# Optimization experiments

Hardware: AMD Instinct MI355X
Metric: run time of the kernel (lower is better)

Reference implementation:

```python
import jax, jax.numpy as jnp
import numpy as np

N_NODES = 50000
N_EDGES = 800000
D_IN = 256
D_OUT = 256


def setup_inputs() -> dict:
    key = jax.random.key(0)
    ks = jax.random.split(key, 8)
    x = jax.random.normal(ks[0], (N_NODES, D_IN), dtype=jnp.float32)
    edge_index = jax.random.randint(ks[1], (2, N_EDGES), 0, N_NODES, dtype=jnp.int64)
    W_src = jax.random.normal(ks[2], (D_IN, D_OUT), dtype=jnp.float32) * 0.05
    b_src = jax.random.normal(ks[3], (D_OUT,), dtype=jnp.float32) * 0.05
    W_dst = jax.random.normal(ks[4], (D_IN, D_OUT), dtype=jnp.float32) * 0.05
    b_dst = jax.random.normal(ks[5], (D_OUT,), dtype=jnp.float32) * 0.05
    W_self = jax.random.normal(ks[6], (D_IN, D_OUT), dtype=jnp.float32) * 0.05
    b_self = jax.random.normal(ks[7], (D_OUT,), dtype=jnp.float32) * 0.05
    return {"x": x, "edge_index": edge_index, "W_src": W_src, "b_src": b_src,
            "W_dst": W_dst, "b_dst": b_dst, "W_self": W_self, "b_self": b_self}


def reference(x, edge_index, W_src, b_src, W_dst, b_dst, W_self, b_self):
    # LEConv: messages = src_linear(x[row]) - dst_linear(x[col]);
    # scatter-add messages into destination nodes (col); add self_linear(x).
    # Linear commutes with row-gather, so project once on [N, d] then gather.
    row, col = edge_index[0], edge_index[1]
    src = x @ W_src + b_src            # [N, D_OUT]
    dst = x @ W_dst + b_dst            # [N, D_OUT]
    messages = src[row] - dst[col]     # [E, D_OUT]
    agg = jax.ops.segment_sum(messages, col, num_segments=x.shape[0])  # [N, D_OUT]
    return x @ W_self + b_self + agg
```

## Files before the change

kernel.cpp:

```cpp
#include <hip/hip_runtime.h>

#define D 256

typedef unsigned short ushort_t;
typedef unsigned int uint_t;
typedef __attribute__((ext_vector_type(8))) short short8;
typedef __attribute__((ext_vector_type(4))) float floatx4;

static __device__ __forceinline__ ushort_t f2bf(float f) {
    union { float f; uint_t u; } c; c.f = f;
    uint_t r = (c.u + 0x7FFFu + ((c.u >> 16) & 1u)) >> 16;
    return (ushort_t)r;
}
static __device__ __forceinline__ float bf2f(ushort_t b) {
    union { uint_t u; float f; } c; c.u = ((uint_t)b) << 16;
    return c.f;
}

static __device__ __forceinline__ void async16(const void* g, void* l) {
    __builtin_amdgcn_global_load_lds(
        (const __attribute__((address_space(1))) void*)g,
        (__attribute__((address_space(3))) void*)l, 16, 0, 0);
}

__global__ void prep_kernel(const int* __restrict__ col, int* __restrict__ deg,
                            int* __restrict__ rank,
                            const float* __restrict__ x, ushort_t* __restrict__ xh,
                            const float* __restrict__ Wself, const float* __restrict__ Wsrc,
                            const float* __restrict__ Wdst, ushort_t* __restrict__ BT,
                            int E, int total8, int degB, int cvtB) {
    int b = blockIdx.x;
    if (b < degB) {
        int e = b * 256 + threadIdx.x;
        if (e < E) rank[e] = atomicAdd(&deg[col[e]], 1);
    } else if (b < degB + cvtB) {
        int i = (b - degB) * 256 + threadIdx.x;
        if (i >= total8) return;
        float4 a = ((const float4*)x)[i * 2];
        float4 bb = ((const float4*)x)[i * 2 + 1];
        uint4 o;
        o.x = f2bf(a.x) | ((uint_t)f2bf(a.y) << 16);
        o.y = f2bf(a.z) | ((uint_t)f2bf(a.w) << 16);
        o.z = f2bf(bb.x) | ((uint_t)f2bf(bb.y) << 16);
        o.w = f2bf(bb.z) | ((uint_t)f2bf(bb.w) << 16);
        ((uint4*)xh)[i] = o;
    } else {
        int id = (b - degB - cvtB) * 256 + threadIdx.x;
        if (id >= 256 * 768) return;
        int j = id / 768, k = id % 768;
        float v;
        if (k < 256)      v = Wself[(size_t)k * 256 + j];
        else if (k < 512) v = Wsrc [(size_t)(k - 256) * 256 + j];
        else              v = Wdst [(size_t)(k - 512) * 256 + j];
        BT[id] = f2bf(v);
    }
}

__global__ __launch_bounds__(256) void scanA(const int* __restrict__ deg,
                                             int* __restrict__ off,
                                             int* __restrict__ partials, int n4) {
    __shared__ int wtot[4];
    const int tid = threadIdx.x, lane = tid & 63, wid = tid >> 6;
    int i4 = blockIdx.x * 256 + tid;
    int4 v = (i4 < n4) ? ((const int4*)deg)[i4] : make_int4(0, 0, 0, 0);
    int s = v.x + v.y + v.z + v.w;
    int incl = s;
    #pragma unroll
    for (int st = 1; st < 64; st <<= 1) {
        int t = __shfl_up(incl, st, 64);
        if (lane >= st) incl += t;
    }
    if (lane == 63) wtot[wid] = incl;
    __syncthreads();
    int wbase = 0;
    #pragma unroll
    for (int w = 0; w < 4; ++w) if (w < wid) wbase += wtot[w];
    int excl = incl - s + wbase;
    if (i4 < n4) {
        int4 o;
        o.x = excl; o.y = o.x + v.x; o.z = o.y + v.y; o.w = o.z + v.z;
        ((int4*)off)[i4] = o;
    }
    if (tid == 0) partials[blockIdx.x] = wtot[0] + wtot[1] + wtot[2] + wtot[3];
}

__global__ __launch_bounds__(256) void scanC(int* __restrict__ off,
                                             const int* __restrict__ partials, int n4) {
    __shared__ int base_s;
    const int tid = threadIdx.x;
    if (tid < 64) {
        int v = (tid < blockIdx.x) ? partials[tid] : 0;
        #pragma unroll
        for (int st = 32; st; st >>= 1) v += __shfl_down(v, st, 64);
        if (tid == 0) base_s = v;
    }
    __syncthreads();
    int base = base_s;
    int i4 = blockIdx.x * 256 + tid;
    if (i4 < n4) {
        int4 o = ((int4*)off)[i4];
        o.x += base; o.y += base; o.z += base; o.w += base;
        ((int4*)off)[i4] = o;
    }
}

__global__ void fill_kernel(const int* __restrict__ row, const int* __restrict__ col,
                            const int* __restrict__ rank, const int* __restrict__ off,
                            int* __restrict__ bucket, int E) {
    int e = blockIdx.x * blockDim.x + threadIdx.x;
    if (e >= E) return;
    bucket[off[col[e]] + rank[e]] = row[e];
}

__global__ __launch_bounds__(256) void segsum_kernel(const ushort_t* __restrict__ xh,
                                                     const int* __restrict__ off,
                                                     const int* __restrict__ deg,
                                                     const int* __restrict__ bucket,
                                                     ushort_t* __restrict__ Gh, int N) {
    int node = blockIdx.x * 4 + (threadIdx.x >> 6);
    int lane = threadIdx.x & 63;
    if (node >= N) return;
    int start = off[node];
    int cnt = deg[node];
    float a0 = 0.f, a1 = 0.f, a2 = 0.f, a3 = 0.f;
    int i = 0;
    for (; i + 4 <= cnt; i += 4) {
        int r0 = bucket[start + i];
        int r1 = bucket[start + i + 1];
        int r2 = bucket[start + i + 2];
        int r3 = bucket[start + i + 3];
        ushort4 v0 = ((const ushort4*)(xh + (size_t)r0 * D))[lane];
        ushort4 v1 = ((const ushort4*)(xh + (size_t)r1 * D))[lane];
        ushort4 v2 = ((const ushort4*)(xh + (size_t)r2 * D))[lane];
        ushort4 v3 = ((const ushort4*)(xh + (size_t)r3 * D))[lane];
        a0 += (bf2f(v0.x) + bf2f(v1.x)) + (bf2f(v2.x) + bf2f(v3.x));
        a1 += (bf2f(v0.y) + bf2f(v1.y)) + (bf2f(v2.y) + bf2f(v3.y));
        a2 += (bf2f(v0.z) + bf2f(v1.z)) + (bf2f(v2.z) + bf2f(v3.z));
        a3 += (bf2f(v0.w) + bf2f(v1.w)) + (bf2f(v2.w) + bf2f(v3.w));
    }
    for (; i < cnt; ++i) {
        int r0 = bucket[start + i];
        ushort4 v0 = ((const ushort4*)(xh + (size_t)r0 * D))[lane];
        a0 += bf2f(v0.x); a1 += bf2f(v0.y); a2 += bf2f(v0.z); a3 += bf2f(v0.w);
    }
    ushort4 o;
    o.x = f2bf(a0); o.y = f2bf(a1); o.z = f2bf(a2); o.w = f2bf(a3);
    ((ushort4*)(Gh + (size_t)node * D))[lane] = o;
}

__global__ __launch_bounds__(256, 2) void mfma_gemm(
    const ushort_t* __restrict__ xh, const ushort_t* __restrict__ Gh,
    const ushort_t* __restrict__ BT, const int* __restrict__ deg,
    const float* __restrict__ bsrc, const float* __restrict__ bdst,
    const float* __restrict__ bself, float* __restrict__ out, int N)
{
    __shared__ ushort_t Bs[2][16][64][8];
    __shared__ ushort_t Bd[2][16][64][8];

    const int tid = threadIdx.x;
    const int lane = tid & 63, wave = tid >> 6;
    const int quad = lane >> 4, l15 = lane & 15;
    const int wr = wave >> 1, wc = wave & 1;
    const int mbase = blockIdx.x * 128;

    size_t aoff[4];
    float negdeg[4];
    #pragma unroll
    for (int im = 0; im < 4; ++im) {
        int r = mbase + wr * 64 + im * 16 + l15;
        if (r >= N) r = N - 1;
        aoff[im] = (size_t)r * 256 + (size_t)(quad * 8);
        negdeg[im] = -(float)deg[r];
    }

    const ushort_t* bpg[4];
    #pragma unroll
    for (int t = 0; t < 4; ++t)
        bpg[t] = BT + (size_t)((wave * 4 + t) * 16 + l15) * 768 + quad * 8;

    floatx4 acc[4][8] = {};
    short8 af[2][4];

    auto issueB = [&](int s) {
        const int b = s & 1;
        if (s < 8) {
            const int kb = s * 32;
            #pragma unroll
            for (int t = 0; t < 4; ++t)
                async16(bpg[t] + kb, &Bs[b][wave * 4 + t][0][0]);
            #pragma unroll
            for (int t = 0; t < 4; ++t)
                async16(bpg[t] + 512 + kb, &Bd[b][wave * 4 + t][0][0]);
        } else {
            const int kb = 256 + (s - 8) * 32;
            #pragma unroll
            for (int t = 0; t < 4; ++t)
                async16(bpg[t] + kb, &Bs[b][wave * 4 + t][0][0]);
        }
    };
    auto loadA = [&](int s) {
        const ushort_t* Ap = (s < 8) ? xh : Gh;
        const int ka = (s & 7) * 32;
        #pragma unroll
        for (int im = 0; im < 4; ++im)
            af[s & 1][im] = *(const short8*)(Ap + aoff[im] + ka);
    };

    issueB(0);
    loadA(0);

    #pragma unroll
    for (int s = 0; s < 16; ++s) {
        const int cur = s & 1;

        if (s < 15) { issueB(s + 1); loadA(s + 1); }

        if (s < 7)        asm volatile("s_waitcnt vmcnt(12)" ::: "memory");
        else if (s < 15)  asm volatile("s_waitcnt vmcnt(8)"  ::: "memory");
        else              asm volatile("s_waitcnt vmcnt(0)"  ::: "memory");
        __builtin_amdgcn_s_barrier();

        #pragma unroll
        for (int jn = 0; jn < 8; ++jn) {
            short8 bf = *(const short8*)(&Bs[cur][wc * 8 + jn][lane][0]);
            #pragma unroll
            for (int im = 0; im < 4; ++im)
                acc[im][jn] = __builtin_amdgcn_mfma_f32_16x16x32_bf16(
                    af[cur][im], bf, acc[im][jn], 0, 0, 0);
        }
        if (s < 8) {
            short8 afd[4];
            #pragma unroll
            for (int im = 0; im < 4; ++im) {
                short8 t = af[cur][im];
                #pragma unroll
                for (int j = 0; j < 8; ++j) {
                    float f = bf2f((ushort_t)t[j]) * negdeg[im];
                    t[j] = (short)f2bf(f);
                }
                afd[im] = t;
            }
            #pragma unroll
            for (int jn = 0; jn < 8; ++jn) {
                short8 bf = *(const short8*)(&Bd[cur][wc * 8 + jn][lane][0]);
                #pragma unroll
                for (int im = 0; im < 4; ++im)
                    acc[im][jn] = __builtin_amdgcn_mfma_f32_16x16x32_bf16(
                        afd[im], bf, acc[im][jn], 0, 0, 0);
            }
        }

        if (s < 15) __builtin_amdgcn_s_barrier();
    }

    float degv[4][4];
    #pragma unroll
    for (int im = 0; im < 4; ++im)
        #pragma unroll
        for (int r = 0; r < 4; ++r) {
            int gm = mbase + wr * 64 + im * 16 + quad * 4 + r;
            degv[im][r] = (gm < N) ? (float)deg[gm] : 0.f;
        }

    #pragma unroll
    for (int jn = 0; jn < 8; ++jn) {
        int gn = wc * 128 + jn * 16 + l15;
        float bs = bself[gn];
        float db = bsrc[gn] - bdst[gn];
        #pragma unroll
        for (int im = 0; im < 4; ++im) {
            #pragma unroll
            for (int r = 0; r < 4; ++r) {
                int gm = mbase + wr * 64 + im * 16 + quad * 4 + r;
                if (gm < N) {
                    out[(size_t)gm * 256 + gn] =
                        acc[im][jn][r] + bs + degv[im][r] * db;
                }
            }
        }
    }
}

extern "C" void kernel_launch(void* const* d_in, const int* in_sizes, int n_in,
                              void* d_out, int out_size, void* d_ws, size_t ws_size,
                              hipStream_t stream) {
    const float* x     = (const float*)d_in[0];
    const int*   eidx  = (const int*)d_in[1];
    const float* Wsrc  = (const float*)d_in[2];
    const float* bsrc  = (const float*)d_in[3];
    const float* Wdst  = (const float*)d_in[4];
    const float* bdst  = (const float*)d_in[5];
    const float* Wself = (const float*)d_in[6];
    const float* bself = (const float*)d_in[7];
    float* out = (float*)d_out;

    const int N = in_sizes[0] / D;
    const int E = in_sizes[1] / 2;
    const int* row = eidx;
    const int* col = eidx + E;

    char* p = (char*)d_ws;
    ushort_t* xh  = (ushort_t*)p;        p += (size_t)N * D * sizeof(ushort_t);
    ushort_t* Gh  = (ushort_t*)p;        int* rank = (int*)p;
                                         p += (size_t)N * D * sizeof(ushort_t);
    ushort_t* BT  = (ushort_t*)p;        p += (size_t)768 * 256 * sizeof(ushort_t);
    int* deg      = (int*)p;             p += (size_t)N * sizeof(int);
    int* off      = (int*)p;             p += (size_t)N * sizeof(int);
    int* partials = (int*)p;             p += 64 * sizeof(int);
    int* bucket   = (int*)p;

    hipMemsetAsync(deg, 0, (size_t)N * sizeof(int), stream);

    const int total8 = N * D / 8;
    const int degB = (E + 255) / 256;
    const int cvtB = (total8 + 255) / 256;
    const int btB  = (256 * 768 + 255) / 256;
    prep_kernel<<<degB + cvtB + btB, 256, 0, stream>>>(col, deg, rank, x, xh,
                                                       Wself, Wsrc, Wdst, BT,
                                                       E, total8, degB, cvtB);
    const int n4 = N / 4;
    const int nblk = (n4 + 255) / 256;
    scanA<<<nblk, 256, 0, stream>>>(deg, off, partials, n4);
    scanC<<<nblk, 256, 0, stream>>>(off, partials, n4);
    fill_kernel<<<(E + 255) / 256, 256, 0, stream>>>(row, col, rank, off, bucket, E);
    segsum_kernel<<<(N + 3) / 4, 256, 0, stream>>>(xh, off, deg, bucket, Gh, N);

    mfma_gemm<<<(N + 127) / 128, 256, 0, stream>>>(xh, Gh, BT, deg,
                                                   bsrc, bdst, bself, out, N);
}
```

Measured before the change: 279.2 us.

## Drop LDS staging in GEMM; load B fragments directly from global per wave

The fused GEMM no longer stages weight tiles in shared memory with async global-to-LDS copies and double buffering. Each block now covers 64 rows, and each of the four waves owns a 64-column slice, loading its A and B fragments straight from global memory (relying on L2/L1 for reuse). This removes barriers, LDS traffic and register pressure from the 4x8 accumulator tile, and doubles the grid size for occupancy. In exchange, B is re-read from cache by every block with less reuse per load, and there is no explicit prefetch, so load latency is exposed.

```diff
diff --git a/kernel.cpp b/kernel.cpp
--- a/kernel.cpp
+++ b/kernel.cpp
@@ -15,12 +15,6 @@
 static __device__ __forceinline__ float bf2f(ushort_t b) {
     union { uint_t u; float f; } c; c.u = ((uint_t)b) << 16;
     return c.f;
-}
-
-static __device__ __forceinline__ void async16(const void* g, void* l) {
-    __builtin_amdgcn_global_load_lds(
-        (const __attribute__((address_space(1))) void*)g,
-        (__attribute__((address_space(3))) void*)l, 16, 0, 0);
 }
 
 __global__ void prep_kernel(const int* __restrict__ col, int* __restrict__ deg,
@@ -154,85 +148,59 @@
     const float* __restrict__ bsrc, const float* __restrict__ bdst,
     const float* __restrict__ bself, float* __restrict__ out, int N)
 {
-    __shared__ ushort_t Bs[2][16][64][8];
-    __shared__ ushort_t Bd[2][16][64][8];
-
     const int tid = threadIdx.x;
     const int lane = tid & 63, wave = tid >> 6;
     const int quad = lane >> 4, l15 = lane & 15;
-    const int wr = wave >> 1, wc = wave & 1;
-    const int mbase = blockIdx.x * 128;
+    const int mbase = blockIdx.x * 64;
 
     size_t aoff[4];
     float negdeg[4];
     #pragma unroll
     for (int im = 0; im < 4; ++im) {
-        int r = mbase + wr * 64 + im * 16 + l15;
+        int r = mbase + im * 16 + l15;
         if (r >= N) r = N - 1;
         aoff[im] = (size_t)r * 256 + (size_t)(quad * 8);
         negdeg[im] = -(float)deg[r];
     }
 
-    const ushort_t* bpg[4];
-    #pragma unroll
-    for (int t = 0; t < 4; ++t)
-        bpg[t] = BT + (size_t)((wave * 4 + t) * 16 + l15) * 768 + quad * 8;
-
-    floatx4 acc[4][8] = {};
-    short8 af[2][4];
-
-    auto issueB = [&](int s) {
-        const int b = s & 1;
+    const ushort_t* bp[4];
+    #pragma unroll
+    for (int jn = 0; jn < 4; ++jn)
+        bp[jn] = BT + (size_t)(wave * 64 + jn * 16 + l15) * 768 + quad * 8;
+
+    floatx4 acc[4][4] = {};
+
+    #pragma unroll
+    for (int s = 0; s < 16; ++s) {
+        const ushort_t* Ap = (s < 8) ? xh : Gh;
+        const int ka = (s & 7) * 32;
+
+        short8 af[4];
+        #pragma unroll
+        for (int im = 0; im < 4; ++im)
+            af[im] = *(const short8*)(Ap + aoff[im] + ka);
+
         if (s < 8) {
             const int kb = s * 32;
-            #pragma unroll
-            for (int t = 0; t < 4; ++t)
-                async16(bpg[t] + kb, &Bs[b][wave * 4 + t][0][0]);
-            #pragma unroll
-            for (int t = 0; t < 4; ++t)
-                async16(bpg[t] + 512 + kb, &Bd[b][wave * 4 + t][0][0]);
-        } else {
-            const int kb = 256 + (s - 8) * 32;
-            #pragma unroll
-            for (int t = 0; t < 4; ++t)
-                async16(bpg[t] + kb, &Bs[b][wave * 4 + t][0][0]);
-        }
-    };
-    auto loadA = [&](int s) {
-        const ushort_t* Ap = (s < 8) ? xh : Gh;
-        const int ka = (s & 7) * 32;
-        #pragma unroll
-        for (int im = 0; im < 4; ++im)
-            af[s & 1][im] = *(const short8*)(Ap + aoff[im] + ka);
-    };
-
-    issueB(0);
-    loadA(0);
-
-    #pragma unroll
-    for (int s = 0; s < 16; ++s) {
-        const int cur = s & 1;
-
-        if (s < 15) { issueB(s + 1); loadA(s + 1); }
-
-        if (s < 7)        asm volatile("s_waitcnt vmcnt(12)" ::: "memory");
-        else if (s < 15)  asm volatile("s_waitcnt vmcnt(8)"  ::: "memory");
-        else              asm volatile("s_waitcnt vmcnt(0)"  ::: "memory");
-        __builtin_amdgcn_s_barrier();
-
-        #pragma unroll
-        for (int jn = 0; jn < 8; ++jn) {
-            short8 bf = *(const short8*)(&Bs[cur][wc * 8 + jn][lane][0]);
-            #pragma unroll
-            for (int im = 0; im < 4; ++im)
-                acc[im][jn] = __builtin_amdgcn_mfma_f32_16x16x32_bf16(
-                    af[cur][im], bf, acc[im][jn], 0, 0, 0);
-        }
-        if (s < 8) {
+            short8 bfs[4], bfd[4];
+            #pragma unroll
+            for (int jn = 0; jn < 4; ++jn)
+                bfs[jn] = *(const short8*)(bp[jn] + kb);
+            #pragma unroll
+            for (int jn = 0; jn < 4; ++jn)
+                bfd[jn] = *(const short8*)(bp[jn] + 512 + kb);
+
+            #pragma unroll
+            for (int jn = 0; jn < 4; ++jn)
+                #pragma unroll
+                for (int im = 0; im < 4; ++im)
+                    acc[im][jn] = __builtin_amdgcn_mfma_f32_16x16x32_bf16(
+                        af[im], bfs[jn], acc[im][jn], 0, 0, 0);
+
             short8 afd[4];
             #pragma unroll
             for (int im = 0; im < 4; ++im) {
-                short8 t = af[cur][im];
+                short8 t = af[im];
                 #pragma unroll
                 for (int j = 0; j < 8; ++j) {
                     float f = bf2f((ushort_t)t[j]) * negdeg[im];
@@ -241,16 +209,24 @@
                 afd[im] = t;
             }
             #pragma unroll
-            for (int jn = 0; jn < 8; ++jn) {
-                short8 bf = *(const short8*)(&Bd[cur][wc * 8 + jn][lane][0]);
+            for (int jn = 0; jn < 4; ++jn)
                 #pragma unroll
                 for (int im = 0; im < 4; ++im)
                     acc[im][jn] = __builtin_amdgcn_mfma_f32_16x16x32_bf16(
-                        afd[im], bf, acc[im][jn], 0, 0, 0);
-            }
+                        afd[im], bfd[jn], acc[im][jn], 0, 0, 0);
+        } else {
+            const int kb = 256 + (s - 8) * 32;
+            short8 bfs[4];
+            #pragma unroll
+            for (int jn = 0; jn < 4; ++jn)
+                bfs[jn] = *(const short8*)(bp[jn] + kb);
+            #pragma unroll
+            for (int jn = 0; jn < 4; ++jn)
+                #pragma unroll
+                for (int im = 0; im < 4; ++im)
+                    acc[im][jn] = __builtin_amdgcn_mfma_f32_16x16x32_bf16(
+                        af[im], bfs[jn], acc[im][jn], 0, 0, 0);
         }
-
-        if (s < 15) __builtin_amdgcn_s_barrier();
     }
 
     float degv[4][4];
@@ -258,20 +234,20 @@
     for (int im = 0; im < 4; ++im)
         #pragma unroll
         for (int r = 0; r < 4; ++r) {
-            int gm = mbase + wr * 64 + im * 16 + quad * 4 + r;
+            int gm = mbase + im * 16 + quad * 4 + r;
             degv[im][r] = (gm < N) ? (float)deg[gm] : 0.f;
         }
 
     #pragma unroll
-    for (int jn = 0; jn < 8; ++jn) {
-        int gn = wc * 128 + jn * 16 + l15;
+    for (int jn = 0; jn < 4; ++jn) {
+        int gn = wave * 64 + jn * 16 + l15;
         float bs = bself[gn];
         float db = bsrc[gn] - bdst[gn];
         #pragma unroll
         for (int im = 0; im < 4; ++im) {
             #pragma unroll
             for (int r = 0; r < 4; ++r) {
-                int gm = mbase + wr * 64 + im * 16 + quad * 4 + r;
+                int gm = mbase + im * 16 + quad * 4 + r;
                 if (gm < N) {
                     out[(size_t)gm * 256 + gn] =
                         acc[im][jn][r] + bs + degv[im][r] * db;
@@ -325,6 +301,6 @@
     fill_kernel<<<(E + 255) / 256, 256, 0, stream>>>(row, col, rank, off, bucket, E);
     segsum_kernel<<<(N + 3) / 4, 256, 0, stream>>>(xh, off, deg, bucket, Gh, N);
 
-    mfma_gemm<<<(N + 127) / 128, 256, 0, stream>>>(xh, Gh, BT, deg,
-                                                   bsrc, bdst, bself, out, N);
-}
+    mfma_gemm<<<(N + 63) / 64, 256, 0, stream>>>(xh, Gh, BT, deg,
+                                                 bsrc, bdst, bself, out, N);
+}
```

Result: slower. 307.5 us (+10.1%).
